# Optimization experiments

Hardware: AMD Instinct MI355X
Metric: run time of the kernel (lower is better)

The kernel has to match this reference:

```python
import jax, jax.numpy as jnp
import numpy as np

H, D = 8, 32
IN, HID, OUT = 256, 256, 128
N_PAR, N_FIG, N_TAB, N_CIT = 100000, 20000, 20000, 50000
E = 200000


def setup_inputs() -> dict:
    key = jax.random.key(0)
    ks = iter(jax.random.split(key, 80))
    def nrm(shape, s=0.05):
        return jax.random.normal(next(ks), shape, dtype=jnp.float32) * s
    def ridx(n):
        return jax.random.randint(next(ks), (E,), 0, n, dtype=jnp.int32)
    inp = {
        'x_par': nrm((N_PAR, IN), 1.0), 'x_fig': nrm((N_FIG, IN), 1.0),
        'x_tab': nrm((N_TAB, IN), 1.0), 'x_cit': nrm((N_CIT, IN), 1.0),
    }
    for t in ['par', 'fig', 'tab', 'cit']:
        inp[f'Wp_{t}'] = nrm((IN, HID)); inp[f'bp_{t}'] = nrm((HID,))
    for et in ['pf', 'fp', 'pt', 'tp', 'pc', 'cp']:
        inp[f'a_{et}_s'] = nrm((H, D)); inp[f'a_{et}_d'] = nrm((H, D))
    inp['k_w'] = nrm((HID, HID)); inp['k_b'] = nrm((HID,)); inp['q'] = nrm((HID,))
    for t in ['par', 'fig', 'tab', 'cit']:
        inp[f'Wh_{t}'] = nrm((HID, OUT)); inp[f'bh_{t}'] = nrm((OUT,))
    inp['cls_w'] = nrm((2 * OUT, 1)); inp['cls_b'] = nrm((1,))
    inp['pf_src'] = ridx(N_PAR); inp['pf_dst'] = ridx(N_FIG)
    inp['fp_src'] = ridx(N_FIG); inp['fp_dst'] = ridx(N_PAR)
    inp['pt_src'] = ridx(N_PAR); inp['pt_dst'] = ridx(N_TAB)
    inp['tp_src'] = ridx(N_TAB); inp['tp_dst'] = ridx(N_PAR)
    inp['pc_src'] = ridx(N_PAR); inp['pc_dst'] = ridx(N_CIT)
    inp['cp_src'] = ridx(N_CIT); inp['cp_dst'] = ridx(N_PAR)
    inp['target_node_idx'] = 5
    return inp


def _agg(xs, xd, si, di, a_s, a_d, n_dst):
    # HANConv metapath aggregation: GAT-style attention + per-dst softmax + scatter-sum + relu
    as_ = jnp.einsum('nhd,hd->nh', xs, a_s)            # [Ns,H]
    ad_ = jnp.einsum('nhd,hd->nh', xd, a_d)            # [Nd,H]
    alpha = jax.nn.leaky_relu(as_[si] + ad_[di], 0.2)  # [E,H]
    m = jax.ops.segment_max(alpha, di, num_segments=n_dst)
    m = jnp.where(jnp.isfinite(m), m, 0.0)
    ex = jnp.exp(alpha - m[di])
    den = jax.ops.segment_sum(ex, di, num_segments=n_dst)
    w = ex / (den[di] + 1e-16)
    out = jax.ops.segment_sum(xs[si] * w[:, :, None], di, num_segments=n_dst)  # [Nd,H,D]
    return jax.nn.relu(out.reshape(n_dst, H * D))


def _group(outs, q, kw, kb):
    # HANConv semantic (metapath-level) attention
    st = jnp.stack(outs)                               # [M,N,F]
    kmean = jnp.tanh(st @ kw + kb).mean(axis=1)        # [M,F]
    attn = jax.nn.softmax(kmean @ q)                   # [M]
    return jnp.einsum('m,mnf->nf', attn, st)


def reference(x_par, x_fig, x_tab, x_cit,
              Wp_par, bp_par, Wp_fig, bp_fig, Wp_tab, bp_tab, Wp_cit, bp_cit,
              a_pf_s, a_pf_d, a_fp_s, a_fp_d, a_pt_s, a_pt_d,
              a_tp_s, a_tp_d, a_pc_s, a_pc_d, a_cp_s, a_cp_d,
              k_w, k_b, q,
              Wh_par, bh_par, Wh_fig, bh_fig, Wh_tab, bh_tab, Wh_cit, bh_cit,
              cls_w, cls_b,
              pf_src, pf_dst, fp_src, fp_dst, pt_src, pt_dst,
              tp_src, tp_dst, pc_src, pc_dst, cp_src, cp_dst,
              target_node_idx):
    # per-node-type input projection
    h_par = (x_par @ Wp_par + bp_par).reshape(-1, H, D)
    h_fig = (x_fig @ Wp_fig + bp_fig).reshape(-1, H, D)
    h_tab = (x_tab @ Wp_tab + bp_tab).reshape(-1, H, D)
    h_cit = (x_cit @ Wp_cit + bp_cit).reshape(-1, H, D)
    # per-metapath message passing, grouped per destination node type
    o_fig = _group([_agg(h_par, h_fig, pf_src, pf_dst, a_pf_s, a_pf_d, N_FIG)], q, k_w, k_b)
    o_tab = _group([_agg(h_par, h_tab, pt_src, pt_dst, a_pt_s, a_pt_d, N_TAB)], q, k_w, k_b)
    o_cit = _group([_agg(h_par, h_cit, pc_src, pc_dst, a_pc_s, a_pc_d, N_CIT)], q, k_w, k_b)
    o_par = _group([
        _agg(h_fig, h_par, fp_src, fp_dst, a_fp_s, a_fp_d, N_PAR),
        _agg(h_tab, h_par, tp_src, tp_dst, a_tp_s, a_tp_d, N_PAR),
        _agg(h_cit, h_par, cp_src, cp_dst, a_cp_s, a_cp_d, N_PAR),
    ], q, k_w, k_b)
    # output heads (table/cited_paper heads computed in the original but unused for scores)
    par_emb = o_par @ Wh_par + bh_par
    fig_emb = o_fig @ Wh_fig + bh_fig
    _ = o_tab @ Wh_tab + bh_tab
    _ = o_cit @ Wh_cit + bh_cit
    # pairwise classifier: target figure embedding broadcast against every paragraph
    target = fig_emb[target_node_idx]
    comb = jnp.concatenate(
        [jnp.broadcast_to(target[None, :], (par_emb.shape[0], OUT)), par_emb], axis=1)
    scores = (comb @ cls_w + cls_b)[:, 0]
    return scores
```

## Files before the change

### kernel.cpp

```cpp
#include <hip/hip_runtime.h>
#include <hip/hip_bf16.h>
#include <math.h>

typedef float f32x4 __attribute__((ext_vector_type(4)));
typedef short bf16x8 __attribute__((ext_vector_type(8)));

#define NPAR 100000
#define NFIG 20000
#define NTAB 20000
#define NCIT 50000
#define NEDGE 200000
#define CAP 32
#define MPAD 100096
#define PFCAP 79

__device__ __forceinline__ unsigned short f2b(float f) {
    union { float f; unsigned u; } x; x.f = f;
    unsigned r = x.u + 0x7FFFu + ((x.u >> 16) & 1u);
    return (unsigned short)(r >> 16);
}
__device__ __forceinline__ float b2f(unsigned short b) {
    union { unsigned u; float f; } x; x.u = ((unsigned)b) << 16; return x.f;
}
__device__ __forceinline__ float fast_tanh(float x) {
    float e = __expf(2.f * x);
    return 1.f - 2.f * __builtin_amdgcn_rcpf(e + 1.f);
}
__device__ __forceinline__ void async_copy16(const unsigned short* g, unsigned short* l) {
    __builtin_amdgcn_global_load_lds(
        (const __attribute__((address_space(1))) unsigned int*)g,
        (__attribute__((address_space(3))) unsigned int*)l, 16, 0, 0);
}

__global__ void k_transpose5(const float* __restrict__ W0, const float* __restrict__ W1,
                             const float* __restrict__ W2, const float* __restrict__ W3,
                             const float* __restrict__ W4, unsigned short* __restrict__ WT) {
    int b = blockIdx.x, which = b >> 8, k = b & 255, n = threadIdx.x;
    const float* W = which == 0 ? W0 : which == 1 ? W1 : which == 2 ? W2 : which == 3 ? W3 : W4;
    WT[(size_t)which * 65536 + n * 256 + k] = f2b(W[k * 256 + n]);
}

__global__ void k_precompute(const float* __restrict__ WhF, const float* __restrict__ bhF,
                             const float* __restrict__ WhP, const float* __restrict__ bhP,
                             const float* __restrict__ clsw, const float* __restrict__ clsb,
                             float* __restrict__ u, float* __restrict__ v, float* __restrict__ smallb) {
    int t = threadIdx.x;
    float su = 0.f, sv = 0.f;
    for (int j = 0; j < 128; ++j) {
        su += WhF[t * 128 + j] * clsw[j];
        sv += WhP[t * 128 + j] * clsw[128 + j];
    }
    u[t] = su; v[t] = sv;
    if (t == 0) {
        float c = clsb[0];
        for (int j = 0; j < 128; ++j) c += bhF[j] * clsw[j] + bhP[j] * clsw[128 + j];
        smallb[264] = c;
    }
}

struct ProjPack {
    const float* X[4];
    const unsigned short* WT[4];
    const float* bias[4];
    unsigned short* H[4];
    const float* av[16];
    float* ov[16];
    int nrows[4];
    int bbase[4];
    int nv[4];
};

#define LOADA(k0, A0, A1) do { \
    const float4* _p = reinterpret_cast<const float4*>(Arow + (k0)); \
    A0 = _p[0]; A1 = _p[1]; } while (0)
#define WRITEA(buf, A0, A1) do { \
    __align__(16) unsigned short _t[8]; \
    _t[0] = f2b(A0.x); _t[1] = f2b(A0.y); _t[2] = f2b(A0.z); _t[3] = f2b(A0.w); \
    _t[4] = f2b(A1.x); _t[5] = f2b(A1.y); _t[6] = f2b(A1.z); _t[7] = f2b(A1.w); \
    *reinterpret_cast<uint4*>(&As[buf][arow * 32 + acol]) = *reinterpret_cast<const uint4*>(_t); } while (0)

__global__ __launch_bounds__(512, 4) void k_gemm_proj(ProjPack p) {
    __shared__ __align__(16) unsigned short As[2][128 * 32];
    __shared__ __align__(16) unsigned short Bs[2][256 * 32];
    __shared__ float satt[4][128][8];
    int bid = blockIdx.x;
    int ty = (bid >= p.bbase[1]) + (bid >= p.bbase[2]) + (bid >= p.bbase[3]);
    int m0 = (bid - p.bbase[ty]) * 128;
    const float* Xf = p.X[ty];
    const unsigned short* B = p.WT[ty];
    unsigned short* Hout = p.H[ty];
    int Nrows = p.nrows[ty];
    int nv = p.nv[ty];

    int t = threadIdx.x, l = t & 63, w = t >> 6;
    int wm = (w >> 2) * 64, wn = (w & 3) * 64;
    int lr = l & 15, hi = l >> 4;
    int arow = t >> 2, acol = (t & 3) * 8;
    int arow_c = m0 + arow; if (arow_c > Nrows - 1) arow_c = Nrows - 1;
    const float* Arow = Xf + (size_t)arow_c * 256 + acol;
    f32x4 acc[4][4] = {};
    float4 aP0, aP1, aQ0, aQ1;

    auto stageB = [&](int buf, int k0) {
#pragma unroll
        for (int i = 0; i < 2; ++i) {
            int rowb = w * 32 + i * 16;
            async_copy16(B + (size_t)(rowb + (l >> 2)) * 256 + k0 + (l & 3) * 8,
                         &Bs[buf][rowb * 32]);
        }
    };

    LOADA(0, aP0, aP1);
    stageB(0, 0);
    WRITEA(0, aP0, aP1);
    LOADA(32, aQ0, aQ1);
    asm volatile("s_waitcnt vmcnt(2) lgkmcnt(0)" ::: "memory");
    __builtin_amdgcn_s_barrier();

#pragma unroll
    for (int ks = 0; ks < 8; ++ks) {
        int cur = ks & 1;
        if (ks < 7) stageB(cur ^ 1, (ks + 1) * 32);
        if (ks < 6) {
            if ((ks & 1) == 0) LOADA((ks + 2) * 32, aP0, aP1);
            else               LOADA((ks + 2) * 32, aQ0, aQ1);
        }
        bf16x8 af[4], bfr[4];
#pragma unroll
        for (int mm = 0; mm < 4; ++mm)
            af[mm] = *reinterpret_cast<const bf16x8*>(&As[cur][(wm + mm * 16 + lr) * 32 + hi * 8]);
#pragma unroll
        for (int nn = 0; nn < 4; ++nn)
            bfr[nn] = *reinterpret_cast<const bf16x8*>(&Bs[cur][(wn + nn * 16 + lr) * 32 + hi * 8]);
#pragma unroll
        for (int mm = 0; mm < 4; ++mm)
#pragma unroll
            for (int nn = 0; nn < 4; ++nn)
                acc[mm][nn] = __builtin_amdgcn_mfma_f32_16x16x32_bf16(bfr[nn], af[mm], acc[mm][nn], 0, 0, 0);
        if (ks < 7) {
            if ((ks & 1) == 0) WRITEA(cur ^ 1, aQ0, aQ1);
            else               WRITEA(cur ^ 1, aP0, aP1);
            if (ks < 6) asm volatile("s_waitcnt vmcnt(2) lgkmcnt(0)" ::: "memory");
            else        asm volatile("s_waitcnt vmcnt(0) lgkmcnt(0)" ::: "memory");
            __builtin_amdgcn_s_barrier();
        }
    }

    float4 bv4[4], av4[4][4];
#pragma unroll
    for (int nn = 0; nn < 4; ++nn)
        bv4[nn] = *reinterpret_cast<const float4*>(p.bias[ty] + wn + nn * 16 + hi * 4);
#pragma unroll
    for (int v = 0; v < 4; ++v)
        if (v < nv) {
            const float* A = p.av[ty * 4 + v];
#pragma unroll
            for (int nn = 0; nn < 4; ++nn)
                av4[v][nn] = *reinterpret_cast<const float4*>(A + wn + nn * 16 + hi * 4);
        }
    int h0 = (w & 3) * 2;
#pragma unroll
    for (int mm = 0; mm < 4; ++mm) {
        int lrow = wm + mm * 16 + lr;
        int row = m0 + lrow;
        float sv[4][2] = {};
#pragma unroll
        for (int nn = 0; nn < 4; ++nn) {
            float c0 = acc[mm][nn][0] + bv4[nn].x;
            float c1 = acc[mm][nn][1] + bv4[nn].y;
            float c2 = acc[mm][nn][2] + bv4[nn].z;
            float c3 = acc[mm][nn][3] + bv4[nn].w;
            if (ty != 0 && row < Nrows) {
                ushort4 o; o.x = f2b(c0); o.y = f2b(c1); o.z = f2b(c2); o.w = f2b(c3);
                *reinterpret_cast<ushort4*>(Hout + (size_t)row * 256 + wn + nn * 16 + hi * 4) = o;
            }
#pragma unroll
            for (int v = 0; v < 4; ++v)
                if (v < nv)
                    sv[v][nn >> 1] += c0 * av4[v][nn].x + c1 * av4[v][nn].y +
                                      c2 * av4[v][nn].z + c3 * av4[v][nn].w;
        }
#pragma unroll
        for (int v = 0; v < 4; ++v)
            if (v < nv) {
#pragma unroll
                for (int hp = 0; hp < 2; ++hp) {
                    float s = sv[v][hp];
                    s += __shfl_xor(s, 16); s += __shfl_xor(s, 32);
                    if (hi == 0) satt[v][lrow][h0 + hp] = s;
                }
            }
    }
    __syncthreads();
    for (int i = t; i < nv * 1024; i += 512) {
        int v = i >> 10, rem = i & 1023, lrow = rem >> 3, hd = rem & 7;
        int g = m0 + lrow;
        if (g < Nrows) p.ov[ty * 4 + v][(size_t)g * 8 + hd] = satt[v][lrow][hd];
    }
}

__global__ void k_pf_proj(const int* __restrict__ mlist, const float* __restrict__ Xp,
                          const unsigned short* __restrict__ WTp, const float* __restrict__ bp,
                          unsigned short* __restrict__ Hs) {
    int b = blockIdx.x;
    int cnt = mlist[0]; if (cnt > PFCAP) cnt = PFCAP;
    if (b >= cnt) return;
    int s = mlist[1 + b];
    __shared__ float xr[256];
    int t = threadIdx.x;
    xr[t] = Xp[(size_t)s * 256 + t];
    __syncthreads();
    const unsigned short* wrow = WTp + (size_t)t * 256;
    float acc = bp[t];
    for (int k = 0; k < 256; k += 8) {
        uint4 wv = *reinterpret_cast<const uint4*>(wrow + k);
        unsigned wsv[4] = { wv.x, wv.y, wv.z, wv.w };
#pragma unroll
        for (int j = 0; j < 4; ++j) {
            acc += xr[k + j * 2]     * b2f((unsigned short)(wsv[j] & 0xffffu));
            acc += xr[k + j * 2 + 1] * b2f((unsigned short)(wsv[j] >> 16));
        }
    }
    Hs[(size_t)b * 256 + t] = f2b(acc);
}

__global__ __launch_bounds__(512, 4) void k_gather_kmean(
    const int* __restrict__ src, const int* __restrict__ count,
    const int* __restrict__ elist, const unsigned short* __restrict__ Hsrc,
    const float* __restrict__ as_, const float* __restrict__ ad_,
    const unsigned short* __restrict__ Bw, const float* __restrict__ kb,
    const float* __restrict__ v, float* __restrict__ ksum,
    float* __restrict__ gout) {
    __shared__ __align__(16) unsigned short Ar[64 * 256];
    __shared__ __align__(16) unsigned short Bs[2][256 * 32];
    int t = threadIdx.x, l = t & 63, w = t >> 6;
    int m0 = blockIdx.x * 64;
    int lg = l & 15, gb = l & 48;
    float* ks_rep = ksum + (size_t)(blockIdx.x & 7) * 256;

    auto stageB = [&](int buf, int k0) {
#pragma unroll
        for (int i = 0; i < 2; ++i) {
            int rowb = w * 32 + i * 16;
            async_copy16(Bw + (size_t)(rowb + (l >> 2)) * 256 + k0 + (l & 3) * 8,
                         &Bs[buf][rowb * 32]);
        }
    };
    stageB(0, 0);

    int cnt_[2], s1_[2], s2_[2], ld_[2]; float adh_[2]; bool val_[2];
#pragma unroll
    for (int j = 0; j < 2; ++j) {
        int ld = w * 8 + j * 4 + (l >> 4);
        int d = m0 + ld;
        bool valid = d < NPAR;
        int cnt = 0;
        if (valid) { cnt = count[d]; if (cnt > CAP) cnt = CAP; }
        int e1 = (lg < cnt) ? elist[(size_t)d * CAP + lg] : -1;
        int e2 = (lg + 16 < cnt) ? elist[(size_t)d * CAP + lg + 16] : -1;
        ld_[j] = ld; val_[j] = valid; cnt_[j] = cnt;
        s1_[j] = (e1 >= 0) ? src[e1] : 0;
        s2_[j] = (e2 >= 0) ? src[e2] : 0;
        adh_[j] = valid ? ad_[d * 8 + (lg >> 1)] : 0.f;
    }

    float4 vv0 = *reinterpret_cast<const float4*>(v + lg * 16);
    float4 vv1 = *reinterpret_cast<const float4*>(v + lg * 16 + 4);
    float4 vv2 = *reinterpret_cast<const float4*>(v + lg * 16 + 8);
    float4 vv3 = *reinterpret_cast<const float4*>(v + lg * 16 + 12);
    float vr[16] = { vv0.x, vv0.y, vv0.z, vv0.w, vv1.x, vv1.y, vv1.z, vv1.w,
                     vv2.x, vv2.y, vv2.z, vv2.w, vv3.x, vv3.y, vv3.z, vv3.w };

#pragma unroll
    for (int j = 0; j < 2; ++j) {
        int cnt = cnt_[j], s1 = s1_[j], s2 = s2_[j], ld = ld_[j];
        float adh = adh_[j];
        float ar[16];
#pragma unroll
        for (int k = 0; k < 16; ++k) ar[k] = 0.f;
        float den = 0.f;
        int sC = __shfl(s1, gb);
        const uint4* hp0 = reinterpret_cast<const uint4*>(Hsrc + (size_t)sC * 256 + lg * 16);
        uint4 hA = {}, hB = {};
        float asv = 0.f;
        if (cnt > 0) { hA = hp0[0]; hB = hp0[1]; asv = as_[sC * 8 + (lg >> 1)]; }
        for (int i = 0; i < cnt; ++i) {
            int iN = i + 1;
            uint4 nA = {}, nB = {};
            float nas = 0.f;
            if (iN < cnt) {
                int sN = (iN < 16) ? __shfl(s1, gb + (iN & 15)) : __shfl(s2, gb + ((iN - 16) & 15));
                const uint4* np = reinterpret_cast<const uint4*>(Hsrc + (size_t)sN * 256 + lg * 16);
                nA = np[0]; nB = np[1];
                nas = as_[sN * 8 + (lg >> 1)];
            }
            float al = asv + adh;
            al = al > 0.f ? al : 0.2f * al;
            float ex = __expf(al); den += ex;
            unsigned wds[8] = { hA.x, hA.y, hA.z, hA.w, hB.x, hB.y, hB.z, hB.w };
#pragma unroll
            for (int k = 0; k < 8; ++k) {
                ar[k * 2]     += ex * b2f((unsigned short)(wds[k] & 0xffffu));
                ar[k * 2 + 1] += ex * b2f((unsigned short)(wds[k] >> 16));
            }
            hA = nA; hB = nB; asv = nas;
        }
        float inv = 1.f / (den + 1e-16f);
        float gs = 0.f;
        __align__(16) unsigned short ob[16];
#pragma unroll
        for (int k = 0; k < 16; ++k) {
            float r = fmaxf(ar[k] * inv, 0.f);
            gs += r * vr[k];
            ob[k] = f2b(r);
        }
        int u0 = (lg * 2) ^ (ld & 7), u1 = (lg * 2 + 1) ^ (ld & 7);
        *reinterpret_cast<uint4*>(&Ar[ld * 256 + u0 * 8]) = *reinterpret_cast<const uint4*>(ob);
        *reinterpret_cast<uint4*>(&Ar[ld * 256 + u1 * 8]) = *reinterpret_cast<const uint4*>(ob + 8);
        gs += __shfl_xor(gs, 1); gs += __shfl_xor(gs, 2); gs += __shfl_xor(gs, 4); gs += __shfl_xor(gs, 8);
        if (lg == 0 && val_[j]) gout[m0 + ld] = gs;
    }
    __syncthreads();

    int wm = (w >> 2) * 32, wn = (w & 3) * 64, lr = l & 15, hi = l >> 4;
    f32x4 acc[2][4] = {};
    int cur = 0;
    for (int ks = 0; ks < 8; ++ks) {
        if (ks < 7) stageB(cur ^ 1, (ks + 1) * 32);
        bf16x8 af[2], bfr[4];
#pragma unroll
        for (int mm = 0; mm < 2; ++mm) {
            int rr = wm + mm * 16 + lr;
            af[mm] = *reinterpret_cast<const bf16x8*>(&Ar[rr * 256 + (((ks * 4 + hi) ^ (rr & 7)) * 8)]);
        }
#pragma unroll
        for (int nn = 0; nn < 4; ++nn)
            bfr[nn] = *reinterpret_cast<const bf16x8*>(&Bs[cur][(wn + nn * 16 + lr) * 32 + hi * 8]);
#pragma unroll
        for (int mm = 0; mm < 2; ++mm)
#pragma unroll
            for (int nn = 0; nn < 4; ++nn)
                acc[mm][nn] = __builtin_amdgcn_mfma_f32_16x16x32_bf16(af[mm], bfr[nn], acc[mm][nn], 0, 0, 0);
        __syncthreads();
        cur ^= 1;
    }
#pragma unroll
    for (int nn = 0; nn < 4; ++nn) {
        int col = wn + nn * 16 + lr;
        float kbv = kb[col];
        float cs = 0.f;
#pragma unroll
        for (int mm = 0; mm < 2; ++mm)
#pragma unroll
            for (int r = 0; r < 4; ++r) {
                int row = m0 + wm + mm * 16 + hi * 4 + r;
                if (row < NPAR) cs += fast_tanh(acc[mm][nn][r] + kbv);
            }
        cs += __shfl_xor(cs, 16);
        cs += __shfl_xor(cs, 32);
        if (hi == 0) atomicAdd(&ks_rep[col], cs);
    }
}

__global__ void k_bucket3(const int* __restrict__ d0, const int* __restrict__ d1,
                          const int* __restrict__ d2, int* __restrict__ count,
                          int* __restrict__ elist) {
    int b = blockIdx.x;
    int m = b / 782;
    int e = (b - m * 782) * 256 + threadIdx.x;
    if (e >= NEDGE) return;
    const int* dst = m == 0 ? d0 : m == 1 ? d1 : d2;
    int d = dst[e];
    int* cnt = count + (size_t)m * NPAR;
    int* el = elist + (size_t)m * NPAR * CAP;
    int slot = atomicAdd(&cnt[d], 1);
    if (slot < CAP) el[(size_t)d * CAP + slot] = e;
}

__global__ void k_pf_scan(const int* __restrict__ psrc, const int* __restrict__ pdst,
                          const int* __restrict__ tgtp, int* __restrict__ mlist) {
    int e = blockIdx.x * 256 + threadIdx.x;
    if (e >= NEDGE) return;
    if (pdst[e] == tgtp[0]) {
        int slot = atomicAdd(&mlist[0], 1);
        if (slot < PFCAP) mlist[1 + slot] = psrc[e];
    }
}

__global__ void k_pf_acc(const int* __restrict__ mlist, const int* __restrict__ tgtp,
                         const unsigned short* __restrict__ Hs,
                         const float* __restrict__ as_pf, const float* __restrict__ ad_pf,
                         float* __restrict__ smallb) {
    __shared__ float sacc[4][256];
    __shared__ float sden[4][8];
    int t = threadIdx.x, w = t >> 6, l = t & 63;
    int tgt = tgtp[0];
    int cnt = mlist[0]; if (cnt > PFCAP) cnt = PFCAP;
    int h = l >> 3;
    float adh = ad_pf[tgt * 8 + h];
    float a0 = 0.f, a1 = 0.f, a2 = 0.f, a3 = 0.f, den = 0.f;
    for (int i = w; i < cnt; i += 4) {
        int s = mlist[1 + i];
        float al = as_pf[s * 8 + h] + adh;
        al = al > 0.f ? al : 0.2f * al;
        float ex = __expf(al);
        ushort4 hv = *reinterpret_cast<const ushort4*>(&Hs[(size_t)i * 256 + l * 4]);
        a0 += ex * b2f(hv.x); a1 += ex * b2f(hv.y); a2 += ex * b2f(hv.z); a3 += ex * b2f(hv.w);
        den += ex;
    }
    sacc[w][l * 4 + 0] = a0; sacc[w][l * 4 + 1] = a1;
    sacc[w][l * 4 + 2] = a2; sacc[w][l * 4 + 3] = a3;
    if ((l & 7) == 0) sden[w][h] = den;
    __syncthreads();
    smallb[t] = sacc[0][t] + sacc[1][t] + sacc[2][t] + sacc[3][t];
    if (t < 8) smallb[256 + t] = sden[0][t] + sden[1][t] + sden[2][t] + sden[3][t];
}

__global__ void k_finalize(const float* __restrict__ kacc, const float* __restrict__ q,
                           const float* __restrict__ u, float* __restrict__ smallb) {
    __shared__ float red[256];
    __shared__ float sm[3];
    int t = threadIdx.x;
    float qv = q[t];
    for (int m = 0; m < 3; ++m) {
        float acc = 0.f;
#pragma unroll
        for (int rep = 0; rep < 8; ++rep) acc += kacc[m * 2048 + rep * 256 + t];
        red[t] = acc * qv;
        __syncthreads();
        for (int s = 128; s > 0; s >>= 1) { if (t < s) red[t] += red[t + s]; __syncthreads(); }
        if (t == 0) sm[m] = red[0] / (float)NPAR;
        __syncthreads();
    }
    float den = smallb[256 + (t >> 5)];
    float rt = fmaxf(smallb[t] / (den + 1e-16f), 0.f);
    red[t] = rt * u[t];
    __syncthreads();
    for (int s = 128; s > 0; s >>= 1) { if (t < s) red[t] += red[t + s]; __syncthreads(); }
    if (t == 0) {
        float mx = fmaxf(sm[0], fmaxf(sm[1], sm[2]));
        float e0 = expf(sm[0] - mx), e1 = expf(sm[1] - mx), e2 = expf(sm[2] - mx);
        float sd = e0 + e1 + e2;
        smallb[265] = e0 / sd; smallb[266] = e1 / sd; smallb[267] = e2 / sd;
        smallb[268] = red[0] + smallb[264];
    }
}

__global__ void k_scores(const float* __restrict__ g, const float* __restrict__ smallb,
                         float* __restrict__ out) {
    int i = blockIdx.x * 256 + threadIdx.x;
    if (i >= NPAR) return;
    out[i] = smallb[268] + smallb[265] * g[i] + smallb[266] * g[NPAR + i] + smallb[267] * g[2 * NPAR + i];
}

extern "C" void kernel_launch(void* const* d_in, const int* in_sizes, int n_in,
                              void* d_out, int out_size, void* d_ws, size_t ws_size,
                              hipStream_t stream) {
    char* base = (char*)d_ws;
    size_t off = 0;
    auto alloc = [&](size_t b) -> void* { void* p = base + off; off += (b + 255) & ~(size_t)255; return p; };

    unsigned short* Hsmall = (unsigned short*)alloc((size_t)PFCAP * 256 * 2);
    unsigned short* h_fig = (unsigned short*)alloc((size_t)NFIG * 256 * 2);
    unsigned short* h_tab = (unsigned short*)alloc((size_t)NTAB * 256 * 2);
    unsigned short* h_cit = (unsigned short*)alloc((size_t)NCIT * 256 * 2);
    unsigned short* WTall = (unsigned short*)alloc((size_t)5 * 65536 * 2);
    unsigned short* WT_par = WTall, *WT_fig = WTall + 65536, *WT_tab = WTall + 2 * 65536,
                  *WT_cit = WTall + 3 * 65536, *kwT = WTall + 4 * 65536;
    float* as_pf = (float*)alloc((size_t)NPAR * 8 * 4);
    float* ad_fp = (float*)alloc((size_t)NPAR * 8 * 4);
    float* ad_tp = (float*)alloc((size_t)NPAR * 8 * 4);
    float* ad_cp = (float*)alloc((size_t)NPAR * 8 * 4);
    float* as_fp = (float*)alloc((size_t)NFIG * 8 * 4);
    float* ad_pf = (float*)alloc((size_t)NFIG * 8 * 4);
    float* as_tp = (float*)alloc((size_t)NTAB * 8 * 4);
    float* as_cp = (float*)alloc((size_t)NCIT * 8 * 4);
    float* gbuf  = (float*)alloc((size_t)3 * NPAR * 4);
    int* count3  = (int*)alloc((size_t)3 * NPAR * 4);
    int* elist3  = (int*)alloc((size_t)3 * NPAR * CAP * 4);
    float* kacc  = (float*)alloc((size_t)3 * 8 * 256 * 4);
    float* smallb = (float*)alloc(512 * 4);
    int* mlist   = (int*)alloc((1 + PFCAP) * 4);
    float* uvec  = (float*)alloc(256 * 4);
    float* vvec  = (float*)alloc(256 * 4);

    hipMemsetAsync(kacc, 0, 24576 + 2048 + 512, stream);
    hipMemsetAsync(count3, 0, (size_t)3 * NPAR * 4, stream);

    k_transpose5<<<5 * 256, 256, 0, stream>>>((const float*)d_in[4], (const float*)d_in[6],
                                              (const float*)d_in[8], (const float*)d_in[10],
                                              (const float*)d_in[24], WTall);

    k_precompute<<<1, 256, 0, stream>>>((const float*)d_in[29], (const float*)d_in[30],
                                        (const float*)d_in[27], (const float*)d_in[28],
                                        (const float*)d_in[35], (const float*)d_in[36],
                                        uvec, vvec, smallb);

    k_bucket3<<<3 * 782, 256, 0, stream>>>((const int*)d_in[40], (const int*)d_in[44],
                                           (const int*)d_in[48], count3, elist3);
    k_pf_scan<<<782, 256, 0, stream>>>((const int*)d_in[37], (const int*)d_in[38],
                                       (const int*)d_in[49], mlist);
    k_pf_proj<<<PFCAP, 256, 0, stream>>>(mlist, (const float*)d_in[0], WT_par,
                                         (const float*)d_in[5], Hsmall);

    ProjPack pp;
    pp.X[0] = (const float*)d_in[0]; pp.X[1] = (const float*)d_in[1];
    pp.X[2] = (const float*)d_in[2]; pp.X[3] = (const float*)d_in[3];
    pp.WT[0] = WT_par; pp.WT[1] = WT_fig; pp.WT[2] = WT_tab; pp.WT[3] = WT_cit;
    pp.bias[0] = (const float*)d_in[5]; pp.bias[1] = (const float*)d_in[7];
    pp.bias[2] = (const float*)d_in[9]; pp.bias[3] = (const float*)d_in[11];
    pp.H[0] = h_fig; pp.H[1] = h_fig; pp.H[2] = h_tab; pp.H[3] = h_cit;
    pp.nrows[0] = NPAR; pp.nrows[1] = NFIG; pp.nrows[2] = NTAB; pp.nrows[3] = NCIT;
    pp.bbase[0] = 0; pp.bbase[1] = 782; pp.bbase[2] = 939; pp.bbase[3] = 1096;
    pp.nv[0] = 4; pp.nv[1] = 2; pp.nv[2] = 1; pp.nv[3] = 1;
    for (int i = 0; i < 16; ++i) { pp.av[i] = nullptr; pp.ov[i] = nullptr; }
    pp.av[0] = (const float*)d_in[12]; pp.ov[0] = as_pf;
    pp.av[1] = (const float*)d_in[15]; pp.ov[1] = ad_fp;
    pp.av[2] = (const float*)d_in[19]; pp.ov[2] = ad_tp;
    pp.av[3] = (const float*)d_in[23]; pp.ov[3] = ad_cp;
    pp.av[4] = (const float*)d_in[14]; pp.ov[4] = as_fp;
    pp.av[5] = (const float*)d_in[13]; pp.ov[5] = ad_pf;
    pp.av[8] = (const float*)d_in[18]; pp.ov[8] = as_tp;
    pp.av[12] = (const float*)d_in[22]; pp.ov[12] = as_cp;
    k_gemm_proj<<<1487, 512, 0, stream>>>(pp);

    k_pf_acc<<<1, 256, 0, stream>>>(mlist, (const int*)d_in[49], Hsmall, as_pf, ad_pf, smallb);

    const int* srcs[3] = { (const int*)d_in[39], (const int*)d_in[43], (const int*)d_in[47] };
    const unsigned short* hsrcs[3] = { h_fig, h_tab, h_cit };
    const float* ass[3] = { as_fp, as_tp, as_cp };
    const float* ads[3] = { ad_fp, ad_tp, ad_cp };
    for (int m = 0; m < 3; ++m) {
        k_gather_kmean<<<1563, 512, 0, stream>>>(srcs[m], count3 + (size_t)m * NPAR,
                                                 elist3 + (size_t)m * NPAR * CAP, hsrcs[m],
                                                 ass[m], ads[m], kwT, (const float*)d_in[25],
                                                 vvec, kacc + (size_t)m * 2048,
                                                 gbuf + (size_t)m * NPAR);
    }

    k_finalize<<<1, 256, 0, stream>>>(kacc, (const float*)d_in[26], uvec, smallb);
    k_scores<<<391, 256, 0, stream>>>(gbuf, smallb, (float*)d_out);
}
```

Measured before the change: 361.8 us.

## Merge edge kernels and gather launches, cut LDS for higher occupancy, stage H stores

Fuses the bucket and pf-scan kernels into a single launch, and fuses the three per-metapath gather_kmean launches into one grid that picks its metapath from the block index. Shared memory is trimmed so more blocks fit per CU: the projection GEMM reuses its A/B tiles for the attention scratch, and gather_kmean drops B double buffering in favour of barriers around each stage. The projection GEMM also stages its bf16 H output through swizzled LDS so global writes become coalesced 16-byte row stores. Launch bounds rise from 4 to 6 blocks. The single-buffered B removes copy/compute overlap and adds barriers, and the higher occupancy target may force register spills.

```diff
diff --git a/kernel.cpp b/kernel.cpp
--- a/kernel.cpp
+++ b/kernel.cpp
@@ -11,7 +11,6 @@
 #define NCIT 50000
 #define NEDGE 200000
 #define CAP 32
-#define MPAD 100096
 #define PFCAP 79
 
 __device__ __forceinline__ unsigned short f2b(float f) {
@@ -55,6 +54,30 @@
         float c = clsb[0];
         for (int j = 0; j < 128; ++j) c += bhF[j] * clsw[j] + bhP[j] * clsw[128 + j];
         smallb[264] = c;
+    }
+}
+
+__global__ void k_edges(const int* __restrict__ d0, const int* __restrict__ d1,
+                        const int* __restrict__ d2, int* __restrict__ count,
+                        int* __restrict__ elist,
+                        const int* __restrict__ psrc, const int* __restrict__ pdst,
+                        const int* __restrict__ tgtp, int* __restrict__ mlist) {
+    int b = blockIdx.x;
+    int m = b / 782;
+    int e = (b - m * 782) * 256 + threadIdx.x;
+    if (e >= NEDGE) return;
+    if (m < 3) {
+        const int* dst = m == 0 ? d0 : m == 1 ? d1 : d2;
+        int d = dst[e];
+        int* cnt = count + (size_t)m * NPAR;
+        int* el = elist + (size_t)m * NPAR * CAP;
+        int slot = atomicAdd(&cnt[d], 1);
+        if (slot < CAP) el[(size_t)d * CAP + slot] = e;
+    } else {
+        if (pdst[e] == tgtp[0]) {
+            int slot = atomicAdd(&mlist[0], 1);
+            if (slot < PFCAP) mlist[1 + slot] = psrc[e];
+        }
     }
 }
 
@@ -79,10 +102,9 @@
     _t[4] = f2b(A1.x); _t[5] = f2b(A1.y); _t[6] = f2b(A1.z); _t[7] = f2b(A1.w); \
     *reinterpret_cast<uint4*>(&As[buf][arow * 32 + acol]) = *reinterpret_cast<const uint4*>(_t); } while (0)
 
-__global__ __launch_bounds__(512, 4) void k_gemm_proj(ProjPack p) {
+__global__ __launch_bounds__(512, 6) void k_gemm_proj(ProjPack p) {
     __shared__ __align__(16) unsigned short As[2][128 * 32];
     __shared__ __align__(16) unsigned short Bs[2][256 * 32];
-    __shared__ float satt[4][128][8];
     int bid = blockIdx.x;
     int ty = (bid >= p.bbase[1]) + (bid >= p.bbase[2]) + (bid >= p.bbase[3]);
     int m0 = (bid - p.bbase[ty]) * 128;
@@ -146,6 +168,10 @@
         }
     }
 
+    __syncthreads();
+    float* sattp = (float*)&As[0][0];
+    unsigned short* Hst = &Bs[0][0];
+
     float4 bv4[4], av4[4][4];
 #pragma unroll
     for (int nn = 0; nn < 4; ++nn)
@@ -162,7 +188,6 @@
 #pragma unroll
     for (int mm = 0; mm < 4; ++mm) {
         int lrow = wm + mm * 16 + lr;
-        int row = m0 + lrow;
         float sv[4][2] = {};
 #pragma unroll
         for (int nn = 0; nn < 4; ++nn) {
@@ -170,10 +195,6 @@
             float c1 = acc[mm][nn][1] + bv4[nn].y;
             float c2 = acc[mm][nn][2] + bv4[nn].z;
             float c3 = acc[mm][nn][3] + bv4[nn].w;
-            if (ty != 0 && row < Nrows) {
-                ushort4 o; o.x = f2b(c0); o.y = f2b(c1); o.z = f2b(c2); o.w = f2b(c3);
-                *reinterpret_cast<ushort4*>(Hout + (size_t)row * 256 + wn + nn * 16 + hi * 4) = o;
-            }
 #pragma unroll
             for (int v = 0; v < 4; ++v)
                 if (v < nv)
@@ -187,15 +208,55 @@
                 for (int hp = 0; hp < 2; ++hp) {
                     float s = sv[v][hp];
                     s += __shfl_xor(s, 16); s += __shfl_xor(s, 32);
-                    if (hi == 0) satt[v][lrow][h0 + hp] = s;
+                    if (hi == 0) sattp[v * 1024 + lrow * 8 + h0 + hp] = s;
                 }
             }
     }
-    __syncthreads();
+
+    if (ty != 0) {
+        for (int hf = 0; hf < 2; ++hf) {
+            if ((w >> 2) == hf) {
+#pragma unroll
+                for (int mm = 0; mm < 4; ++mm) {
+                    int lr2 = mm * 16 + lr;
+                    int swz = (lr2 & 7) << 4;
+#pragma unroll
+                    for (int nn = 0; nn < 4; ++nn) {
+                        int colb = (wn + nn * 16 + hi * 4) * 2;
+                        ushort4 o;
+                        o.x = f2b(acc[mm][nn][0] + bv4[nn].x);
+                        o.y = f2b(acc[mm][nn][1] + bv4[nn].y);
+                        o.z = f2b(acc[mm][nn][2] + bv4[nn].z);
+                        o.w = f2b(acc[mm][nn][3] + bv4[nn].w);
+                        *reinterpret_cast<ushort4*>((char*)Hst + lr2 * 512 + (colb ^ swz)) = o;
+                    }
+                }
+            }
+            __syncthreads();
+            {
+                int row = t >> 3;
+                int g = m0 + hf * 64 + row;
+                if (g < Nrows) {
+                    int swz = (row & 7) << 4;
+#pragma unroll
+                    for (int pass = 0; pass < 4; ++pass) {
+                        int c = (t & 7) + pass * 8;
+                        uint4 val = *reinterpret_cast<const uint4*>(
+                            (const char*)Hst + row * 512 + ((c * 16) ^ swz));
+                        *reinterpret_cast<uint4*>(Hout + (size_t)g * 256 + c * 8) = val;
+                    }
+                }
+            }
+            __syncthreads();
+        }
+    } else {
+        __syncthreads();
+    }
+
     for (int i = t; i < nv * 1024; i += 512) {
         int v = i >> 10, rem = i & 1023, lrow = rem >> 3, hd = rem & 7;
         int g = m0 + lrow;
-        if (g < Nrows) p.ov[ty * 4 + v][(size_t)g * 8 + hd] = satt[v][lrow][hd];
+        if (g < Nrows) p.ov[ty * 4 + v][(size_t)g * 8 + hd] = sattp[v * 1024 + lrow * 8 + hd];
     }
 }
 
@@ -224,29 +285,38 @@
     Hs[(size_t)b * 256 + t] = f2b(acc);
 }
 
-__global__ __launch_bounds__(512, 4) void k_gather_kmean(
-    const int* __restrict__ src, const int* __restrict__ count,
-    const int* __restrict__ elist, const unsigned short* __restrict__ Hsrc,
-    const float* __restrict__ as_, const float* __restrict__ ad_,
-    const unsigned short* __restrict__ Bw, const float* __restrict__ kb,
-    const float* __restrict__ v, float* __restrict__ ksum,
-    float* __restrict__ gout) {
+struct GKPack {
+    const int* src[3]; const int* count[3]; const int* elist[3];
+    const unsigned short* H[3]; const float* as_[3]; const float* ad_[3];
+    const unsigned short* Bw; const float* kb; const float* v;
+    float* ksum[3]; float* gout[3];
+};
+__global__ __launch_bounds__(512, 6) void k_gather_kmean(GKPack p) {
     __shared__ __align__(16) unsigned short Ar[64 * 256];
-    __shared__ __align__(16) unsigned short Bs[2][256 * 32];
+    __shared__ __align__(16) unsigned short Bs[256 * 32];
+    int bid = blockIdx.x;
+    int m = bid / 1563, b2 = bid - m * 1563;
+    const int* src = p.src[m];
+    const int* count = p.count[m];
+    const int* elist = p.elist[m];
+    const unsigned short* Hsrc = p.H[m];
+    const float* as_ = p.as_[m];
+    const float* ad_ = p.ad_[m];
+    const unsigned short* Bw = p.Bw;
     int t = threadIdx.x, l = t & 63, w = t >> 6;
-    int m0 = blockIdx.x * 64;
+    int m0 = b2 * 64;
     int lg = l & 15, gb = l & 48;
-    float* ks_rep = ksum + (size_t)(blockIdx.x & 7) * 256;
-
-    auto stageB = [&](int buf, int k0) {
+    float* ks_rep = p.ksum[m] + (size_t)(b2 & 7) * 256;
+
+    auto stageB = [&](int k0) {
 #pragma unroll
         for (int i = 0; i < 2; ++i) {
             int rowb = w * 32 + i * 16;
             async_copy16(Bw + (size_t)(rowb + (l >> 2)) * 256 + k0 + (l & 3) * 8,
-                         &Bs[buf][rowb * 32]);
+                         &Bs[rowb * 32]);
         }
     };
-    stageB(0, 0);
+    stageB(0);
 
     int cnt_[2], s1_[2], s2_[2], ld_[2]; float adh_[2]; bool val_[2];
 #pragma unroll
@@ -264,10 +334,10 @@
         adh_[j] = valid ? ad_[d * 8 + (lg >> 1)] : 0.f;
     }
 
-    float4 vv0 = *reinterpret_cast<const float4*>(v + lg * 16);
-    float4 vv1 = *reinterpret_cast<const float4*>(v + lg * 16 + 4);
-    float4 vv2 = *reinterpret_cast<const float4*>(v + lg * 16 + 8);
-    float4 vv3 = *reinterpret_cast<const float4*>(v + lg * 16 + 12);
+    float4 vv0 = *reinterpret_cast<const float4*>(p.v + lg * 16);
+    float4 vv1 = *reinterpret_cast<const float4*>(p.v + lg * 16 + 4);
+    float4 vv2 = *reinterpret_cast<const float4*>(p.v + lg * 16 + 8);
+    float4 vv3 = *reinterpret_cast<const float4*>(p.v + lg * 16 + 12);
     float vr[16] = { vv0.x, vv0.y, vv0.z, vv0.w, vv1.x, vv1.y, vv1.z, vv1.w,
                      vv2.x, vv2.y, vv2.z, vv2.w, vv3.x, vv3.y, vv3.z, vv3.w };
 
@@ -318,15 +388,18 @@
         *reinterpret_cast<uint4*>(&Ar[ld * 256 + u0 * 8]) = *reinterpret_cast<const uint4*>(ob);
         *reinterpret_cast<uint4*>(&Ar[ld * 256 + u1 * 8]) = *reinterpret_cast<const uint4*>(ob + 8);
         gs += __shfl_xor(gs, 1); gs += __shfl_xor(gs, 2); gs += __shfl_xor(gs, 4); gs += __shfl_xor(gs, 8);
-        if (lg == 0 && val_[j]) gout[m0 + ld] = gs;
+        if (lg == 0 && val_[j]) p.gout[m][m0 + ld] = gs;
     }
     __syncthreads();
 
     int wm = (w >> 2) * 32, wn = (w & 3) * 64, lr = l & 15, hi = l >> 4;
     f32x4 acc[2][4] = {};
-    int cur = 0;
     for (int ks = 0; ks < 8; ++ks) {
-        if (ks < 7) stageB(cur ^ 1, (ks + 1) * 32);
+        if (ks > 0) {
+            __syncthreads();
+            stageB(ks * 32);
+            __syncthreads();
+        }
         bf16x8 af[2], bfr[4];
 #pragma unroll
         for (int mm = 0; mm < 2; ++mm) {
@@ -335,19 +408,17 @@
         }
 #pragma unroll
         for (int nn = 0; nn < 4; ++nn)
-            bfr[nn] = *reinterpret_cast<const bf16x8*>(&Bs[cur][(wn + nn * 16 + lr) * 32 + hi * 8]);
+            bfr[nn] = *reinterpret_cast<const bf16x8*>(&Bs[(wn + nn * 16 + lr) * 32 + hi * 8]);
 #pragma unroll
         for (int mm = 0; mm < 2; ++mm)
 #pragma unroll
             for (int nn = 0; nn < 4; ++nn)
                 acc[mm][nn] = __builtin_amdgcn_mfma_f32_16x16x32_bf16(af[mm], bfr[nn], acc[mm][nn], 0, 0, 0);
-        __syncthreads();
-        cur ^= 1;
     }
 #pragma unroll
     for (int nn = 0; nn < 4; ++nn) {
         int col = wn + nn * 16 + lr;
-        float kbv = kb[col];
+        float kbv = p.kb[col];
         float cs = 0.f;
 #pragma unroll
         for (int mm = 0; mm < 2; ++mm)
@@ -359,31 +430,6 @@
         cs += __shfl_xor(cs, 16);
         cs += __shfl_xor(cs, 32);
         if (hi == 0) atomicAdd(&ks_rep[col], cs);
-    }
-}
-
-__global__ void k_bucket3(const int* __restrict__ d0, const int* __restrict__ d1,
-                          const int* __restrict__ d2, int* __restrict__ count,
-                          int* __restrict__ elist) {
-    int b = blockIdx.x;
-    int m = b / 782;
-    int e = (b - m * 782) * 256 + threadIdx.x;
-    if (e >= NEDGE) return;
-    const int* dst = m == 0 ? d0 : m == 1 ? d1 : d2;
-    int d = dst[e];
-    int* cnt = count + (size_t)m * NPAR;
-    int* el = elist + (size_t)m * NPAR * CAP;
-    int slot = atomicAdd(&cnt[d], 1);
-    if (slot < CAP) el[(size_t)d * CAP + slot] = e;
-}
-
-__global__ void k_pf_scan(const int* __restrict__ psrc, const int* __restrict__ pdst,
-                          const int* __restrict__ tgtp, int* __restrict__ mlist) {
-    int e = blockIdx.x * 256 + threadIdx.x;
-    if (e >= NEDGE) return;
-    if (pdst[e] == tgtp[0]) {
-        int slot = atomicAdd(&mlist[0], 1);
-        if (slot < PFCAP) mlist[1 + slot] = psrc[e];
     }
 }
 
@@ -496,10 +542,10 @@
                                         (const float*)d_in[35], (const float*)d_in[36],
                                         uvec, vvec, smallb);
 
-    k_bucket3<<<3 * 782, 256, 0, stream>>>((const int*)d_in[40], (const int*)d_in[44],
-                                           (const int*)d_in[48], count3, elist3);
-    k_pf_scan<<<782, 256, 0, stream>>>((const int*)d_in[37], (const int*)d_in[38],
-                                       (const int*)d_in[49], mlist);
+    k_edges<<<4 * 782, 256, 0, stream>>>((const int*)d_in[40], (const int*)d_in[44],
+                                         (const int*)d_in[48], count3, elist3,
+                                         (const int*)d_in[37], (const int*)d_in[38],
+                                         (const int*)d_in[49], mlist);
     k_pf_proj<<<PFCAP, 256, 0, stream>>>(mlist, (const float*)d_in[0], WT_par,
                                          (const float*)d_in[5], Hsmall);
 
@@ -526,17 +572,17 @@
 
     k_pf_acc<<<1, 256, 0, stream>>>(mlist, (const int*)d_in[49], Hsmall, as_pf, ad_pf, smallb);
 
-    const int* srcs[3] = { (const int*)d_in[39], (const int*)d_in[43], (const int*)d_in[47] };
-    const unsigned short* hsrcs[3] = { h_fig, h_tab, h_cit };
-    const float* ass[3] = { as_fp, as_tp, as_cp };
-    const float* ads[3] = { ad_fp, ad_tp, ad_cp };
-    for (int m = 0; m < 3; ++m) {
-        k_gather_kmean<<<1563, 512, 0, stream>>>(srcs[m], count3 + (size_t)m * NPAR,
-                                                 elist3 + (size_t)m * NPAR * CAP, hsrcs[m],
-                                                 ass[m], ads[m], kwT, (const float*)d_in[25],
-                                                 vvec, kacc + (size_t)m * 2048,
-                                                 gbuf + (size_t)m * NPAR);
-    }
+    GKPack gk;
+    gk.src[0] = (const int*)d_in[39]; gk.src[1] = (const int*)d_in[43]; gk.src[2] = (const int*)d_in[47];
+    gk.count[0] = count3; gk.count[1] = count3 + NPAR; gk.count[2] = count3 + 2 * NPAR;
+    gk.elist[0] = elist3; gk.elist[1] = elist3 + (size_t)NPAR * CAP; gk.elist[2] = elist3 + (size_t)2 * NPAR * CAP;
+    gk.H[0] = h_fig; gk.H[1] = h_tab; gk.H[2] = h_cit;
+    gk.as_[0] = as_fp; gk.as_[1] = as_tp; gk.as_[2] = as_cp;
+    gk.ad_[0] = ad_fp; gk.ad_[1] = ad_tp; gk.ad_[2] = ad_cp;
+    gk.Bw = kwT; gk.kb = (const float*)d_in[25]; gk.v = vvec;
+    gk.ksum[0] = kacc; gk.ksum[1] = kacc + 2048; gk.ksum[2] = kacc + 4096;
+    gk.gout[0] = gbuf; gk.gout[1] = gbuf + NPAR; gk.gout[2] = gbuf + 2 * NPAR;
+    k_gather_kmean<<<3 * 1563, 512, 0, stream>>>(gk);
 
     k_finalize<<<1, 256, 0, stream>>>(kacc, (const float*)d_in[26], uvec, smallb);
     k_scores<<<391, 256, 0, stream>>>(gbuf, smallb, (float*)d_out);
```

Measured after the change: 698.4 us. 93.0% more time.
